# Performance work log

Hardware: AMD Instinct MI355X
Metric: run time of the kernel (lower is better)

## Reference

```python
import jax, jax.numpy as jnp
from jax import lax
import numpy as np

B, C, H, W = 16, 1024, 56, 56   # batch, inplanes(=planes), spatial
G = 4                           # patch_groups
MS = 7                          # mask_size -> 8x8 pixel patches
MID = C // 4                    # planes // expansion = 256


def setup_inputs() -> dict:
    key = jax.random.key(0)
    k1, k2, k3, k4, k5 = jax.random.split(key, 5)
    x = jax.random.normal(k1, (B, C, H, W), jnp.float32)
    # binary routing mask per (batch, group, patch_row, patch_col)
    mask = jax.random.randint(k2, (B, G, MS, MS), 0, 2).astype(jnp.float32)
    # torch grouped-conv weights, layout OIHW with I = in_ch // groups
    w1 = jax.random.normal(k3, (MID, C // G, 1, 1), jnp.float32) * 0.02
    w2 = jax.random.normal(k4, (MID, MID // G, 3, 3), jnp.float32) * 0.02
    w3 = jax.random.normal(k5, (C, MID // G, 1, 1), jnp.float32) * 0.02
    return {"x": x, "mask": mask, "w1": w1, "w2": w2, "w3": w3}


def _gconv(v, w, pad, g):
    # grouped NCHW conv, stride 1, like F.conv2d(..., groups=g)
    return lax.conv_general_dilated(
        v, w, (1, 1), [(pad, pad), (pad, pad)],
        dimension_numbers=("NCHW", "OIHW", "NCHW"),
        feature_group_count=g)


def reference(x, mask, w1, w2, w3):
    b, c, h, w_ = x.shape
    g, ms = mask.shape[1], mask.shape[2]
    cpg = c // g          # channels per group
    hp = h // ms          # pixels per patch side
    # patchify: [b,c,h,w] -> [b,g,cpg,ms,hp,ms,hp] -> patches as batch dim
    # [b*ms*ms, g*cpg, hp, hp]; grouped conv applies each group's weight
    # slice to its channel slab, matching the per-group weight slicing in
    # calc_one_group. padding=1 on conv2 is PER-PATCH (zero pad at patch
    # boundary), exactly as the dispatched inference path computes it.
    xp = x.reshape(b, g, cpg, ms, hp, ms, hp)
    xp = xp.transpose(0, 3, 5, 1, 2, 4, 6).reshape(b * ms * ms, c, hp, hp)
    o = jax.nn.relu(_gconv(xp, w1, 0, g))   # 1x1
    o = jax.nn.relu(_gconv(o, w2, 1, g))    # 3x3, per-patch pad 1
    o = _gconv(o, w3, 0, g)                 # 1x1 -> c_out = planes
    cout = w3.shape[0]
    cog = cout // g
    o = o.reshape(b, ms, ms, g, cog, hp, hp)
    # zero out non-selected patches (combine/scatter step)
    m = (mask > 0).astype(o.dtype).transpose(0, 2, 3, 1)  # [b,ms,ms,g]
    o = o * m[:, :, :, :, None, None, None]
    # un-patchify back to [b, cout, h, w]
    out = o.transpose(0, 3, 4, 1, 5, 2, 6).reshape(b, cout, ms * hp, ms * hp)
    out = out + x  # residual (downsample=None, inplanes==planes)
    return jax.nn.relu(out)  # last_relu=True
```

## Files before the change

### kernel.cpp

```cpp
#include <hip/hip_runtime.h>


typedef __attribute__((ext_vector_type(8))) short bfrag;
typedef __attribute__((ext_vector_type(8))) unsigned short us8;
typedef __attribute__((ext_vector_type(4))) float f4;

__device__ __forceinline__ float bf2f(unsigned short u) {
    union { unsigned int i; float f; } v; v.i = ((unsigned int)u) << 16; return v.f;
}
__device__ __forceinline__ unsigned short f2bf(float f) {
    union { float f; unsigned int i; } v; v.f = f;
    unsigned int u = v.i;
    return (unsigned short)((u + 0x7FFFu + ((u >> 16) & 1u)) >> 16);
}

#define XT_S 264
#define W1_S 136
#define S72  72
#define R2_OFF 16896
#define R3_OFF 26112

__global__ __launch_bounds__(256, 2)
void bottleneck_kernel(const float* __restrict__ x,
                       const float* __restrict__ mask,
                       const float* __restrict__ w1,
                       const float* __restrict__ w2,
                       const float* __restrict__ w3,
                       float* __restrict__ out) {
    __shared__ __align__(16) unsigned short lds[35328];
    unsigned short* XT  = lds;
    unsigned short* R2  = lds + R2_OFF;
    unsigned short* W2s = lds + R3_OFF;
    unsigned short* Y2s = lds + R3_OFF;

    const int tid = threadIdx.x;
    int bid = blockIdx.x;
    const int g = bid & 3;
    int p = bid >> 2;
    const int pc = p % 7; p /= 7;
    const int pr = p % 7;
    const int b  = p / 7;

    const float mval = mask[((b * 4 + g) * 7 + pr) * 7 + pc];
    const size_t xbase = (size_t)(b * 1024 + g * 256) * 3136
                       + (size_t)(pr * 8) * 56 + (size_t)(pc * 8);

    if (mval <= 0.f) {
        for (int k = 0; k < 8; k++) {
            int v = tid + k * 256;
            int ch = v >> 3, py = v & 7;
            size_t off = xbase + (size_t)ch * 3136 + (size_t)py * 56;
            float4 d0 = *(const float4*)(x + off);
            float4 d1 = *(const float4*)(x + off + 4);
            d0.x = fmaxf(d0.x, 0.f); d0.y = fmaxf(d0.y, 0.f);
            d0.z = fmaxf(d0.z, 0.f); d0.w = fmaxf(d0.w, 0.f);
            d1.x = fmaxf(d1.x, 0.f); d1.y = fmaxf(d1.y, 0.f);
            d1.z = fmaxf(d1.z, 0.f); d1.w = fmaxf(d1.w, 0.f);
            *(float4*)(out + off)     = d0;
            *(float4*)(out + off + 4) = d1;
        }
        return;
    }

    const int lane = tid & 63;
    const int wv   = tid >> 6;
    const int l15  = lane & 15;
    const int quad = lane >> 4;
    const int mrow = wv * 16 + l15;
    const int crow = wv * 16 + quad * 4;
    const int cpy  = crow >> 3, cpx0 = crow & 7;

    for (int k = 0; k < 4; k++) {
        int v = tid + k * 256;
        int py = v & 7, chp = v >> 3;
        int ch = chp * 2;
        const float* s0 = x + xbase + (size_t)ch * 3136 + (size_t)py * 56;
        const float* s1 = s0 + 3136;
        float4 a0 = *(const float4*)s0, a1 = *(const float4*)(s0 + 4);
        float4 b0 = *(const float4*)s1, b1 = *(const float4*)(s1 + 4);
        float af[8] = {a0.x,a0.y,a0.z,a0.w,a1.x,a1.y,a1.z,a1.w};
        float bg[8] = {b0.x,b0.y,b0.z,b0.w,b1.x,b1.y,b1.z,b1.w};
        int row0 = py * 8;
#pragma unroll
        for (int px = 0; px < 8; px++) {
            unsigned int u = (unsigned int)f2bf(af[px])
                           | ((unsigned int)f2bf(bg[px]) << 16);
            *(unsigned int*)&XT[(row0 + px) * XT_S + ch] = u;
        }
    }
    {
        int oc = tid & 63, ic0 = (tid >> 6) * 32;
        const float* ws = w1 + (size_t)(g * 64 + oc) * 256 + ic0;
#pragma unroll
        for (int j = 0; j < 4; j++) {
            float4 f0 = *(const float4*)(ws + j * 8);
            float4 f1 = *(const float4*)(ws + j * 8 + 4);
            us8 o;
            o[0]=f2bf(f0.x); o[1]=f2bf(f0.y); o[2]=f2bf(f0.z); o[3]=f2bf(f0.w);
            o[4]=f2bf(f1.x); o[5]=f2bf(f1.y); o[6]=f2bf(f1.z); o[7]=f2bf(f1.w);
            *(us8*)&R2[oc * W1_S + ic0 + j * 8] = o;
        }
    }
    __syncthreads();

    f4 acc1[4];
#pragma unroll
    for (int nt = 0; nt < 4; nt++) acc1[nt] = (f4){0.f, 0.f, 0.f, 0.f};

    for (int h = 0; h < 2; h++) {
        if (h) {
            __syncthreads();
            int oc = tid & 63, ic0 = (tid >> 6) * 32;
            const float* ws = w1 + (size_t)(g * 64 + oc) * 256 + 128 + ic0;
#pragma unroll
            for (int j = 0; j < 4; j++) {
                float4 f0 = *(const float4*)(ws + j * 8);
                float4 f1 = *(const float4*)(ws + j * 8 + 4);
                us8 o;
                o[0]=f2bf(f0.x); o[1]=f2bf(f0.y); o[2]=f2bf(f0.z); o[3]=f2bf(f0.w);
                o[4]=f2bf(f1.x); o[5]=f2bf(f1.y); o[6]=f2bf(f1.z); o[7]=f2bf(f1.w);
                *(us8*)&R2[oc * W1_S + ic0 + j * 8] = o;
            }
            __syncthreads();
        }
#pragma unroll
        for (int ks = 0; ks < 4; ks++) {
            bfrag a = *(const bfrag*)&XT[mrow * XT_S + h * 128 + ks * 32 + quad * 8];
#pragma unroll
            for (int nt = 0; nt < 4; nt++) {
                bfrag bb = *(const bfrag*)&R2[(nt * 16 + l15) * W1_S + ks * 32 + quad * 8];
                acc1[nt] = __builtin_amdgcn_mfma_f32_16x16x32_bf16(a, bb, acc1[nt], 0, 0, 0);
            }
        }
    }
    __syncthreads();

    for (int i = tid; i < 36 * 72; i += 256) {
        int j = i / 72, c = i - j * 72;
        int r = (j < 10) ? j : (j < 20 ? 80 + j
                                       : 10 + ((j - 20) >> 1) * 10 + ((j - 20) & 1) * 9);
        R2[r * S72 + c] = 0;
    }
#pragma unroll
    for (int nt = 0; nt < 4; nt++)
#pragma unroll
        for (int r = 0; r < 4; r++) {
            int px = crow + r;
            int rowp = ((px >> 3) + 1) * 10 + (px & 7) + 1;
            float v = acc1[nt][r]; v = v > 0.f ? v : 0.f;
            R2[rowp * S72 + nt * 16 + l15] = f2bf(v);
        }
    {
        int oc = tid & 63, ic0 = (tid >> 6) * 16;
        const float* ws = w2 + ((size_t)(g * 64 + oc) * 64 + ic0) * 9;
        float t[16];
#pragma unroll
        for (int j = 0; j < 16; j++) t[j] = ws[(size_t)j * 9];
        us8 o0, o1;
#pragma unroll
        for (int j = 0; j < 8; j++) { o0[j] = f2bf(t[j]); o1[j] = f2bf(t[j + 8]); }
        *(us8*)&W2s[oc * S72 + ic0]     = o0;
        *(us8*)&W2s[oc * S72 + ic0 + 8] = o1;
    }
    __syncthreads();

    f4 acc2[4];
#pragma unroll
    for (int nt = 0; nt < 4; nt++) acc2[nt] = (f4){0.f, 0.f, 0.f, 0.f};
    const int apy = mrow >> 3, apx = mrow & 7;

    for (int tap = 0; tap < 9; tap++) {
        const int buf = (tap & 1) * 4608;
        float t[16];
        int oc = tid & 63, ic0 = (tid >> 6) * 16;
        if (tap < 8) {
            const float* ws = w2 + ((size_t)(g * 64 + oc) * 64 + ic0) * 9 + tap + 1;
#pragma unroll
            for (int j = 0; j < 16; j++) t[j] = ws[(size_t)j * 9];
        }
        const int rowp = (apy + tap / 3) * 10 + apx + tap % 3;
#pragma unroll
        for (int ks = 0; ks < 2; ks++) {
            bfrag a = *(const bfrag*)&R2[rowp * S72 + ks * 32 + quad * 8];
#pragma unroll
            for (int nt = 0; nt < 4; nt++) {
                bfrag bb = *(const bfrag*)&W2s[buf + (nt * 16 + l15) * S72 + ks * 32 + quad * 8];
                acc2[nt] = __builtin_amdgcn_mfma_f32_16x16x32_bf16(a, bb, acc2[nt], 0, 0, 0);
            }
        }
        if (tap < 8) {
            us8 o0, o1;
#pragma unroll
            for (int j = 0; j < 8; j++) { o0[j] = f2bf(t[j]); o1[j] = f2bf(t[j + 8]); }
            int nb = 4608 - buf;
            *(us8*)&W2s[nb + oc * S72 + ic0]     = o0;
            *(us8*)&W2s[nb + oc * S72 + ic0 + 8] = o1;
        }
        __syncthreads();
    }

#pragma unroll
    for (int nt = 0; nt < 4; nt++)
#pragma unroll
        for (int r = 0; r < 4; r++) {
            int px = crow + r;
            float v = acc2[nt][r]; v = v > 0.f ? v : 0.f;
            Y2s[px * S72 + nt * 16 + l15] = f2bf(v);
        }
    {
        int ocl = tid & 127, ic0 = (tid >> 7) * 32;
        const float* ws = w3 + (size_t)(g * 256 + ocl) * 64 + ic0;
#pragma unroll
        for (int j = 0; j < 4; j++) {
            float4 f0 = *(const float4*)(ws + j * 8);
            float4 f1 = *(const float4*)(ws + j * 8 + 4);
            us8 o;
            o[0]=f2bf(f0.x); o[1]=f2bf(f0.y); o[2]=f2bf(f0.z); o[3]=f2bf(f0.w);
            o[4]=f2bf(f1.x); o[5]=f2bf(f1.y); o[6]=f2bf(f1.z); o[7]=f2bf(f1.w);
            *(us8*)&R2[ocl * S72 + ic0 + j * 8] = o;
        }
    }
    __syncthreads();

    for (int hh = 0; hh < 2; hh++) {
        if (hh) {
            __syncthreads();
            int ocl = tid & 127, ic0 = (tid >> 7) * 32;
            const float* ws = w3 + (size_t)(g * 256 + 128 + ocl) * 64 + ic0;
#pragma unroll
            for (int j = 0; j < 4; j++) {
                float4 f0 = *(const float4*)(ws + j * 8);
                float4 f1 = *(const float4*)(ws + j * 8 + 4);
                us8 o;
                o[0]=f2bf(f0.x); o[1]=f2bf(f0.y); o[2]=f2bf(f0.z); o[3]=f2bf(f0.w);
                o[4]=f2bf(f1.x); o[5]=f2bf(f1.y); o[6]=f2bf(f1.z); o[7]=f2bf(f1.w);
                *(us8*)&R2[ocl * S72 + ic0 + j * 8] = o;
            }
            __syncthreads();
        }
        f4 acc3[8];
#pragma unroll
        for (int nt = 0; nt < 8; nt++) acc3[nt] = (f4){0.f, 0.f, 0.f, 0.f};
#pragma unroll
        for (int ks = 0; ks < 2; ks++) {
            bfrag a = *(const bfrag*)&Y2s[mrow * S72 + ks * 32 + quad * 8];
#pragma unroll
            for (int nt = 0; nt < 8; nt++) {
                bfrag bb = *(const bfrag*)&R2[(nt * 16 + l15) * S72 + ks * 32 + quad * 8];
                acc3[nt] = __builtin_amdgcn_mfma_f32_16x16x32_bf16(a, bb, acc3[nt], 0, 0, 0);
            }
        }
#pragma unroll
        for (int nt = 0; nt < 8; nt++) {
            int oc = hh * 128 + nt * 16 + l15;
            float4 ov;
            float r0 = acc3[nt][0] + bf2f(XT[(crow + 0) * XT_S + oc]);
            float r1 = acc3[nt][1] + bf2f(XT[(crow + 1) * XT_S + oc]);
            float r2 = acc3[nt][2] + bf2f(XT[(crow + 2) * XT_S + oc]);
            float r3 = acc3[nt][3] + bf2f(XT[(crow + 3) * XT_S + oc]);
            ov.x = fmaxf(r0, 0.f); ov.y = fmaxf(r1, 0.f);
            ov.z = fmaxf(r2, 0.f); ov.w = fmaxf(r3, 0.f);
            *(float4*)(out + xbase + (size_t)oc * 3136 + (size_t)cpy * 56 + cpx0) = ov;
        }
    }
}

extern "C" void kernel_launch(void* const* d_in, const int* in_sizes, int n_in,
                              void* d_out, int out_size, void* d_ws, size_t ws_size,
                              hipStream_t stream) {
    const float* x    = (const float*)d_in[0];
    const float* mask = (const float*)d_in[1];
    const float* w1   = (const float*)d_in[2];
    const float* w2   = (const float*)d_in[3];
    const float* w3   = (const float*)d_in[4];
    float* out = (float*)d_out;

    bottleneck_kernel<<<dim3(16 * 7 * 7 * 4), dim3(256), 0, stream>>>(
        x, mask, w1, w2, w3, out);
}
```

Baseline: 487.1 us.

## Pre-convert weights to bf16 once and read MFMA operands directly from global

Adds a prep kernel that converts w1/w2/w3 to bf16 in a workspace buffer, with w2 re-laid out per tap. The main kernel now loads weight fragments straight from global/L2 into registers instead of staging converted weights through LDS. This removes the per-block conversions and most syncthreads, and it double-buffers the w2 taps in registers. LDS shrinks so occupancy can rise to 4 blocks per CU, and the residual is re-read from x in fp32 rather than taken from bf16 LDS. The cost is an extra kernel launch, more global traffic per block for weights (which should mostly hit cache), and higher register pressure.

After: 570.3 us. 17.1% more time.

```diff
diff --git a/kernel.cpp b/kernel.cpp
--- a/kernel.cpp
+++ b/kernel.cpp
@@ -2,36 +2,42 @@
 
 
 typedef __attribute__((ext_vector_type(8))) short bfrag;
-typedef __attribute__((ext_vector_type(8))) unsigned short us8;
 typedef __attribute__((ext_vector_type(4))) float f4;
 
-__device__ __forceinline__ float bf2f(unsigned short u) {
-    union { unsigned int i; float f; } v; v.i = ((unsigned int)u) << 16; return v.f;
-}
 __device__ __forceinline__ unsigned short f2bf(float f) {
     union { float f; unsigned int i; } v; v.f = f;
     unsigned int u = v.i;
     return (unsigned short)((u + 0x7FFFu + ((u >> 16) & 1u)) >> 16);
 }
 
+__global__ __launch_bounds__(256)
+void prep_weights(const float* __restrict__ w1, const float* __restrict__ w2,
+                  const float* __restrict__ w3, unsigned short* __restrict__ wb) {
+    int i = blockIdx.x * 256 + threadIdx.x;
+    if (i < 65536) {
+        wb[i] = f2bf(w1[i]);
+    } else if (i < 212992) {
+        int j = i - 65536;
+        int ic = j & 63, ocl = (j >> 6) & 63, gt = j >> 12;
+        int tap = gt % 9, g = gt / 9;
+        wb[i] = f2bf(w2[(size_t)((g * 64 + ocl) * 64 + ic) * 9 + tap]);
+    } else {
+        wb[i] = f2bf(w3[i - 212992]);
+    }
+}
+
 #define XT_S 264
-#define W1_S 136
 #define S72  72
-#define R2_OFF 16896
-#define R3_OFF 26112
-
-__global__ __launch_bounds__(256, 2)
+
+__global__ __launch_bounds__(256, 4)
 void bottleneck_kernel(const float* __restrict__ x,
                        const float* __restrict__ mask,
-                       const float* __restrict__ w1,
-                       const float* __restrict__ w2,
-                       const float* __restrict__ w3,
+                       const unsigned short* __restrict__ wbuf,
                        float* __restrict__ out) {
-    __shared__ __align__(16) unsigned short lds[35328];
-    unsigned short* XT  = lds;
-    unsigned short* R2  = lds + R2_OFF;
-    unsigned short* W2s = lds + R3_OFF;
-    unsigned short* Y2s = lds + R3_OFF;
+    __shared__ __align__(16) unsigned short lds[16896];
+    unsigned short* XT = lds;
+    unsigned short* Y1 = lds;
+    unsigned short* Y2 = lds + 7200;
 
     const int tid = threadIdx.x;
     int bid = blockIdx.x;
@@ -88,49 +94,28 @@
             *(unsigned int*)&XT[(row0 + px) * XT_S + ch] = u;
         }
     }
-    {
-        int oc = tid & 63, ic0 = (tid >> 6) * 32;
-        const float* ws = w1 + (size_t)(g * 64 + oc) * 256 + ic0;
-#pragma unroll
-        for (int j = 0; j < 4; j++) {
-            float4 f0 = *(const float4*)(ws + j * 8);
-            float4 f1 = *(const float4*)(ws + j * 8 + 4);
-            us8 o;
-            o[0]=f2bf(f0.x); o[1]=f2bf(f0.y); o[2]=f2bf(f0.z); o[3]=f2bf(f0.w);
-            o[4]=f2bf(f1.x); o[5]=f2bf(f1.y); o[6]=f2bf(f1.z); o[7]=f2bf(f1.w);
-            *(us8*)&R2[oc * W1_S + ic0 + j * 8] = o;
-        }
-    }
-    __syncthreads();
-
+    __syncthreads();
+
+    const unsigned short* W1g = wbuf + (size_t)g * 16384;
     f4 acc1[4];
 #pragma unroll
     for (int nt = 0; nt < 4; nt++) acc1[nt] = (f4){0.f, 0.f, 0.f, 0.f};
-
+#pragma unroll
     for (int h = 0; h < 2; h++) {
-        if (h) {
-            __syncthreads();
-            int oc = tid & 63, ic0 = (tid >> 6) * 32;
-            const float* ws = w1 + (size_t)(g * 64 + oc) * 256 + 128 + ic0;
-#pragma unroll
-            for (int j = 0; j < 4; j++) {
-                float4 f0 = *(const float4*)(ws + j * 8);
-                float4 f1 = *(const float4*)(ws + j * 8 + 4);
-                us8 o;
-                o[0]=f2bf(f0.x); o[1]=f2bf(f0.y); o[2]=f2bf(f0.z); o[3]=f2bf(f0.w);
-                o[4]=f2bf(f1.x); o[5]=f2bf(f1.y); o[6]=f2bf(f1.z); o[7]=f2bf(f1.w);
-                *(us8*)&R2[oc * W1_S + ic0 + j * 8] = o;
-            }
-            __syncthreads();
-        }
 #pragma unroll
         for (int ks = 0; ks < 4; ks++) {
-            bfrag a = *(const bfrag*)&XT[mrow * XT_S + h * 128 + ks * 32 + quad * 8];
-#pragma unroll
-            for (int nt = 0; nt < 4; nt++) {
-                bfrag bb = *(const bfrag*)&R2[(nt * 16 + l15) * W1_S + ks * 32 + quad * 8];
-                acc1[nt] = __builtin_amdgcn_mfma_f32_16x16x32_bf16(a, bb, acc1[nt], 0, 0, 0);
-            }
+            const int koff = h * 128 + ks * 32 + quad * 8;
+            bfrag a = *(const bfrag*)&XT[mrow * XT_S + koff];
+            bfrag b0 = *(const bfrag*)&W1g[0 * 4096 + l15 * 256 + koff];
+            bfrag b1 = *(const bfrag*)&W1g[1 * 4096 + l15 * 256 + koff];
+            bfrag b2 = *(const bfrag*)&W1g[2 * 4096 + l15 * 256 + koff];
+            bfrag b3 = *(const bfrag*)&W1g[3 * 4096 + l15 * 256 + koff];
+            __builtin_amdgcn_s_setprio(1);
+            acc1[0] = __builtin_amdgcn_mfma_f32_16x16x32_bf16(a, b0, acc1[0], 0, 0, 0);
+            acc1[1] = __builtin_amdgcn_mfma_f32_16x16x32_bf16(a, b1, acc1[1], 0, 0, 0);
+            acc1[2] = __builtin_amdgcn_mfma_f32_16x16x32_bf16(a, b2, acc1[2], 0, 0, 0);
+            acc1[3] = __builtin_amdgcn_mfma_f32_16x16x32_bf16(a, b3, acc1[3], 0, 0, 0);
+            __builtin_amdgcn_s_setprio(0);
         }
     }
     __syncthreads();
@@ -139,7 +124,7 @@
         int j = i / 72, c = i - j * 72;
         int r = (j < 10) ? j : (j < 20 ? 80 + j
                                        : 10 + ((j - 20) >> 1) * 10 + ((j - 20) & 1) * 9);
-        R2[r * S72 + c] = 0;
+        Y1[r * S72 + c] = 0;
     }
 #pragma unroll
     for (int nt = 0; nt < 4; nt++)
@@ -148,56 +133,44 @@
             int px = crow + r;
             int rowp = ((px >> 3) + 1) * 10 + (px & 7) + 1;
             float v = acc1[nt][r]; v = v > 0.f ? v : 0.f;
-            R2[rowp * S72 + nt * 16 + l15] = f2bf(v);
-        }
-    {
-        int oc = tid & 63, ic0 = (tid >> 6) * 16;
-        const float* ws = w2 + ((size_t)(g * 64 + oc) * 64 + ic0) * 9;
-        float t[16];
-#pragma unroll
-        for (int j = 0; j < 16; j++) t[j] = ws[(size_t)j * 9];
-        us8 o0, o1;
-#pragma unroll
-        for (int j = 0; j < 8; j++) { o0[j] = f2bf(t[j]); o1[j] = f2bf(t[j + 8]); }
-        *(us8*)&W2s[oc * S72 + ic0]     = o0;
-        *(us8*)&W2s[oc * S72 + ic0 + 8] = o1;
-    }
-    __syncthreads();
-
+            Y1[rowp * S72 + nt * 16 + l15] = f2bf(v);
+        }
+    __syncthreads();
+
+    const unsigned short* W2g = wbuf + 65536 + (size_t)g * 36864;
+    const int w2off = l15 * 64 + quad * 8;
+    const int apy = mrow >> 3, apx = mrow & 7;
     f4 acc2[4];
 #pragma unroll
     for (int nt = 0; nt < 4; nt++) acc2[nt] = (f4){0.f, 0.f, 0.f, 0.f};
-    const int apy = mrow >> 3, apx = mrow & 7;
-
-    for (int tap = 0; tap < 9; tap++) {
-        const int buf = (tap & 1) * 4608;
-        float t[16];
-        int oc = tid & 63, ic0 = (tid >> 6) * 16;
-        if (tap < 8) {
-            const float* ws = w2 + ((size_t)(g * 64 + oc) * 64 + ic0) * 9 + tap + 1;
-#pragma unroll
-            for (int j = 0; j < 16; j++) t[j] = ws[(size_t)j * 9];
-        }
-        const int rowp = (apy + tap / 3) * 10 + apx + tap % 3;
-#pragma unroll
-        for (int ks = 0; ks < 2; ks++) {
-            bfrag a = *(const bfrag*)&R2[rowp * S72 + ks * 32 + quad * 8];
-#pragma unroll
-            for (int nt = 0; nt < 4; nt++) {
-                bfrag bb = *(const bfrag*)&W2s[buf + (nt * 16 + l15) * S72 + ks * 32 + quad * 8];
-                acc2[nt] = __builtin_amdgcn_mfma_f32_16x16x32_bf16(a, bb, acc2[nt], 0, 0, 0);
-            }
-        }
-        if (tap < 8) {
-            us8 o0, o1;
-#pragma unroll
-            for (int j = 0; j < 8; j++) { o0[j] = f2bf(t[j]); o1[j] = f2bf(t[j + 8]); }
-            int nb = 4608 - buf;
-            *(us8*)&W2s[nb + oc * S72 + ic0]     = o0;
-            *(us8*)&W2s[nb + oc * S72 + ic0 + 8] = o1;
-        }
-        __syncthreads();
-    }
+    bfrag wA[8], wB[8];
+
+#define LOADW2(DST, TAP) { \
+    const unsigned short* tw = W2g + (TAP) * 4096 + w2off; \
+    _Pragma("unroll") \
+    for (int i = 0; i < 8; i++) \
+        DST[i] = *(const bfrag*)&tw[(i & 3) * 1024 + (i >> 2) * 32]; }
+
+#define TAP(T, WC, WN) { \
+    if ((T) < 8) LOADW2(WN, (T) + 1); \
+    const int rowp = (apy + (T) / 3) * 10 + apx + (T) % 3; \
+    bfrag a0 = *(const bfrag*)&Y1[rowp * S72 + quad * 8]; \
+    bfrag a1 = *(const bfrag*)&Y1[rowp * S72 + 32 + quad * 8]; \
+    __builtin_amdgcn_s_setprio(1); \
+    _Pragma("unroll") \
+    for (int nt = 0; nt < 4; nt++) \
+        acc2[nt] = __builtin_amdgcn_mfma_f32_16x16x32_bf16(a0, WC[nt], acc2[nt], 0, 0, 0); \
+    _Pragma("unroll") \
+    for (int nt = 0; nt < 4; nt++) \
+        acc2[nt] = __builtin_amdgcn_mfma_f32_16x16x32_bf16(a1, WC[4 + nt], acc2[nt], 0, 0, 0); \
+    __builtin_amdgcn_s_setprio(0); }
+
+    LOADW2(wA, 0);
+    TAP(0, wA, wB); TAP(1, wB, wA); TAP(2, wA, wB);
+    TAP(3, wB, wA); TAP(4, wA, wB); TAP(5, wB, wA);
+    TAP(6, wA, wB); TAP(7, wB, wA); TAP(8, wA, wB);
+#undef TAP
+#undef LOADW2
 
 #pragma unroll
     for (int nt = 0; nt < 4; nt++)
@@ -205,62 +178,39 @@
         for (int r = 0; r < 4; r++) {
             int px = crow + r;
             float v = acc2[nt][r]; v = v > 0.f ? v : 0.f;
-            Y2s[px * S72 + nt * 16 + l15] = f2bf(v);
-        }
-    {
-        int ocl = tid & 127, ic0 = (tid >> 7) * 32;
-        const float* ws = w3 + (size_t)(g * 256 + ocl) * 64 + ic0;
-#pragma unroll
-        for (int j = 0; j < 4; j++) {
-            float4 f0 = *(const float4*)(ws + j * 8);
-            float4 f1 = *(const float4*)(ws + j * 8 + 4);
-            us8 o;
-            o[0]=f2bf(f0.x); o[1]=f2bf(f0.y); o[2]=f2bf(f0.z); o[3]=f2bf(f0.w);
-            o[4]=f2bf(f1.x); o[5]=f2bf(f1.y); o[6]=f2bf(f1.z); o[7]=f2bf(f1.w);
-            *(us8*)&R2[ocl * S72 + ic0 + j * 8] = o;
-        }
-    }
-    __syncthreads();
-
+            Y2[px * S72 + nt * 16 + l15] = f2bf(v);
+        }
+    __syncthreads();
+
+    const unsigned short* W3g = wbuf + 212992 + (size_t)g * 16384;
+#pragma unroll
     for (int hh = 0; hh < 2; hh++) {
-        if (hh) {
-            __syncthreads();
-            int ocl = tid & 127, ic0 = (tid >> 7) * 32;
-            const float* ws = w3 + (size_t)(g * 256 + 128 + ocl) * 64 + ic0;
-#pragma unroll
-            for (int j = 0; j < 4; j++) {
-                float4 f0 = *(const float4*)(ws + j * 8);
-                float4 f1 = *(const float4*)(ws + j * 8 + 4);
-                us8 o;
-                o[0]=f2bf(f0.x); o[1]=f2bf(f0.y); o[2]=f2bf(f0.z); o[3]=f2bf(f0.w);
-                o[4]=f2bf(f1.x); o[5]=f2bf(f1.y); o[6]=f2bf(f1.z); o[7]=f2bf(f1.w);
-                *(us8*)&R2[ocl * S72 + ic0 + j * 8] = o;
-            }
-            __syncthreads();
-        }
         f4 acc3[8];
 #pragma unroll
         for (int nt = 0; nt < 8; nt++) acc3[nt] = (f4){0.f, 0.f, 0.f, 0.f};
 #pragma unroll
         for (int ks = 0; ks < 2; ks++) {
-            bfrag a = *(const bfrag*)&Y2s[mrow * S72 + ks * 32 + quad * 8];
+            bfrag a = *(const bfrag*)&Y2[mrow * S72 + ks * 32 + quad * 8];
+            __builtin_amdgcn_s_setprio(1);
 #pragma unroll
             for (int nt = 0; nt < 8; nt++) {
-                bfrag bb = *(const bfrag*)&R2[(nt * 16 + l15) * S72 + ks * 32 + quad * 8];
+                bfrag bb = *(const bfrag*)&W3g[(hh * 128 + nt * 16 + l15) * 64
+                                               + ks * 32 + quad * 8];
                 acc3[nt] = __builtin_amdgcn_mfma_f32_16x16x32_bf16(a, bb, acc3[nt], 0, 0, 0);
             }
+            __builtin_amdgcn_s_setprio(0);
         }
 #pragma unroll
         for (int nt = 0; nt < 8; nt++) {
             int oc = hh * 128 + nt * 16 + l15;
+            size_t off = xbase + (size_t)oc * 3136 + (size_t)cpy * 56 + cpx0;
+            float4 rv = *(const float4*)(x + off);
             float4 ov;
-            float r0 = acc3[nt][0] + bf2f(XT[(crow + 0) * XT_S + oc]);
-            float r1 = acc3[nt][1] + bf2f(XT[(crow + 1) * XT_S + oc]);
-            float r2 = acc3[nt][2] + bf2f(XT[(crow + 2) * XT_S + oc]);
-            float r3 = acc3[nt][3] + bf2f(XT[(crow + 3) * XT_S + oc]);
-            ov.x = fmaxf(r0, 0.f); ov.y = fmaxf(r1, 0.f);
-            ov.z = fmaxf(r2, 0.f); ov.w = fmaxf(r3, 0.f);
-            *(float4*)(out + xbase + (size_t)oc * 3136 + (size_t)cpy * 56 + cpx0) = ov;
+            ov.x = fmaxf(acc3[nt][0] + rv.x, 0.f);
+            ov.y = fmaxf(acc3[nt][1] + rv.y, 0.f);
+            ov.z = fmaxf(acc3[nt][2] + rv.z, 0.f);
+            ov.w = fmaxf(acc3[nt][3] + rv.w, 0.f);
+            *(float4*)(out + off) = ov;
         }
     }
 }
@@ -274,7 +224,9 @@
     const float* w2   = (const float*)d_in[3];
     const float* w3   = (const float*)d_in[4];
     float* out = (float*)d_out;
-
+    unsigned short* wbuf = (unsigned short*)d_ws;
+
+    prep_weights<<<dim3(1088), dim3(256), 0, stream>>>(w1, w2, w3, wbuf);
     bottleneck_kernel<<<dim3(16 * 7 * 7 * 4), dim3(256), 0, stream>>>(
-        x, mask, w1, w2, w3, out);
-}
+        x, mask, wbuf, out);
+}
```
